# Performance work log

Measured on AMD Instinct MI355X. Metric: run time of the kernel, lower is better.

Reference implementation:

```python
import jax, jax.numpy as jnp
import numpy as np

C = 512          # pc_feat_dim == model_channels
NPTS = 5000      # points per sample (hard-coded in source reshape)
BO = 32          # number of samples
P = 20           # parts per sample (all valid)
S = BO * P       # total valid parts / segments = 640
PPP = (BO * NPTS) // S   # points per part = 250
T = BO * NPTS    # total points = 160000
NUM_FREQS = 10


def setup_inputs() -> dict:
    key = jax.random.key(0)
    ks = jax.random.split(key, 16)
    w = lambda k, shp: (jax.random.normal(k, shp, jnp.float32) * 0.02)
    return {
        "noise_param": jax.random.normal(ks[0], (S, 7), jnp.float32),
        "timesteps": jax.random.randint(ks[1], (BO,), 0, 1000, dtype=jnp.int32),
        "part_pcs": jax.random.normal(ks[2], (T, 3), jnp.float32),
        "segment_ids": (jnp.arange(T, dtype=jnp.int32) // PPP),
        "batch_length": jnp.full((S,), PPP, dtype=jnp.int32),
        "pe_w": w(ks[3], (3, C)), "pe_b": jnp.zeros((C,), jnp.float32),
        "t_w1": w(ks[4], (C, C)), "t_b1": jnp.zeros((C,), jnp.float32),
        "t_w2": w(ks[5], (C, C)), "t_b2": jnp.zeros((C,), jnp.float32),
        "pfc_w": w(ks[6], (147, C)), "pfc_b": jnp.zeros((C,), jnp.float32),
        "o_w1": w(ks[7], (C, 256)), "o_b1": jnp.zeros((256,), jnp.float32),
        "bn1_g": jnp.ones((256,), jnp.float32), "bn1_b": jnp.zeros((256,), jnp.float32),
        "o_w2": w(ks[8], (256, 128)), "o_b2": jnp.zeros((128,), jnp.float32),
        "bn2_g": jnp.ones((128,), jnp.float32), "bn2_b": jnp.zeros((128,), jnp.float32),
        "o_w3": w(ks[9], (128, 7)), "o_b3": jnp.zeros((7,), jnp.float32),
    }


def quat_apply(q, p):
    # pytorch3d convention: quaternion real-part-first (w, x, y, z)
    w, v = q[..., :1], q[..., 1:]
    t = 2.0 * jnp.cross(v, p)
    return p + w * t + jnp.cross(v, t)


def timestep_embedding(t, dim):
    half = dim // 2
    freqs = jnp.exp(-jnp.log(10000.0) * jnp.arange(half, dtype=jnp.float32) / half)
    args = t.astype(jnp.float32)[:, None] * freqs[None, :]
    return jnp.concatenate([jnp.cos(args), jnp.sin(args)], axis=-1)


def nerf_embed(x):
    # include_input, log-sampled freqs 2^0..2^9, fns (sin, cos) -> 7*(1+20)=147
    bands = 2.0 ** jnp.arange(NUM_FREQS, dtype=jnp.float32)
    xb = x[:, None, :] * bands[None, :, None]              # [S, F, 7]
    sc = jnp.concatenate([jnp.sin(xb), jnp.cos(xb)], -1)   # [S, F, 14]
    return jnp.concatenate([x, sc.reshape(x.shape[0], -1)], axis=-1)  # [S, 147]


def batchnorm(x, g, b):
    # training-mode BatchNorm1d over batch dim, eps 1e-5 (biased variance)
    m = x.mean(axis=0)
    v = x.var(axis=0)
    return (x - m) * jax.lax.rsqrt(v + 1e-5) * g + b


def reference(noise_param, timesteps, part_pcs, segment_ids, batch_length,
              pe_w, pe_b, t_w1, t_b1, t_w2, t_b2, pfc_w, pfc_b,
              o_w1, o_b1, bn1_g, bn1_b, o_w2, o_b2, bn2_g, bn2_b, o_w3, o_b3):
    # per-part quaternion + translation, applied per-point via gather
    quat = noise_param[:, 3:]
    quat = quat / jnp.linalg.norm(quat, axis=-1, keepdims=True)
    trans = noise_param[:, :3]
    pts = quat_apply(quat[segment_ids], part_pcs) + trans[segment_ids]  # [T, 3]

    # time embedding MLP (Linear -> SiLU -> Linear), per sample
    temb = timestep_embedding(timesteps, C)
    temb = jax.nn.silu(temb @ t_w1 + t_b1) @ t_w2 + t_b2                # [BO, C]

    feats = pts @ pe_w + pe_b                                           # [T, C]
    point_batch = jnp.arange(T, dtype=jnp.int32) // NPTS
    feats = feats + temb[point_batch]

    # per-part param embedding broadcast-added to that part's points
    pemb = nerf_embed(noise_param) @ pfc_w + pfc_b                      # [S, C]
    feats = feats + pemb[segment_ids]

    # (PointTransformer self/cross layers treated as identity)

    # ragged segment mean pooling
    pooled = jax.ops.segment_sum(feats, segment_ids, num_segments=S)
    pooled = pooled / batch_length[:, None].astype(pooled.dtype)        # [S, C]

    # out head (dropout off)
    h = jax.nn.relu(batchnorm(pooled @ o_w1 + o_b1, bn1_g, bn1_b))
    h = jax.nn.relu(batchnorm(h @ o_w2 + o_b2, bn2_g, bn2_b))
    return h @ o_w3 + o_b3                                              # [S, 7]
```

## Files before the change

kernel.cpp:

```cpp
#include <hip/hip_runtime.h>
#include <math.h>

#define NF 147
#define NBP 152

__global__ __launch_bounds__(256) void k1(
    const float* __restrict__ noise, const int* __restrict__ tsteps,
    const float* __restrict__ pcs, const int* __restrict__ bl,
    const float* __restrict__ t_w1, const float* __restrict__ t_b1,
    const float* __restrict__ t_w2, const float* __restrict__ t_b2,
    const float* __restrict__ pe_w, const float* __restrict__ pe_b,
    const float* __restrict__ pfc_w, const float* __restrict__ pfc_b,
    const float* __restrict__ o_w1,
    float* __restrict__ h1, float* __restrict__ WM, float* __restrict__ nb,
    int* __restrict__ statsz)
{
    __shared__ float shm[6144];
    __shared__ float np7s[4][8];
    __shared__ float wsum[4][3];
    __shared__ float rms[4][3];
    int blk = blockIdx.x, tid = threadIdx.x;

    if (blk < 128) {
        int b = blk >> 2, jq = blk & 3;
        float tf = (float)tsteps[b];
        float f = expf(-9.210340371976184f * (float)tid * (1.f / 256.f));
        float sn, cs;
        sincosf(tf * f, &sn, &cs);
        shm[tid] = cs; shm[256 + tid] = sn;
        __syncthreads();
        int jj = tid & 127, j = jq * 128 + jj;
        int ks = tid >> 7, k0 = ks << 8;
        float acc = 0.f;
        #pragma unroll 8
        for (int k = k0; k < k0 + 256; k++) acc += shm[k] * t_w1[k * 512 + j];
        shm[512 + ks * 128 + jj] = acc;
        __syncthreads();
        if (tid < 128) {
            float v = shm[512 + tid] + shm[640 + tid] + t_b1[jq * 128 + tid];
            h1[b * 512 + jq * 128 + tid] = v / (1.f + expf(-v));
        }
    } else if (blk < 294) {
        int m = blk - 128, r4 = m * 4;
        float* srcs = shm;
        float* red  = shm + 2048;
        #pragma unroll
        for (int q = 0; q < 2; q++) {
            int idx = tid + q * 256;
            int row = idx >> 7;
            int off4 = (idx & 127) << 2;
            int kr = r4 + row;
            float4 v;
            if (kr < 512)      v = *(const float4*)&t_w2[(size_t)kr * 512 + off4];
            else if (kr < 659) v = *(const float4*)&pfc_w[(size_t)(kr - 512) * 512 + off4];
            else if (kr < 662) v = *(const float4*)&pe_w[(size_t)(kr - 659) * 512 + off4];
            else if (kr == 662) {
                float4 a = *(const float4*)&pe_b[off4];
                float4 bq = *(const float4*)&pfc_b[off4];
                v.x = a.x + bq.x; v.y = a.y + bq.y; v.z = a.z + bq.z; v.w = a.w + bq.w;
            } else v = *(const float4*)&t_b2[off4];
            *(float4*)&srcs[row * 512 + off4] = v;
        }
        __syncthreads();
        int ks = tid >> 6, c4 = (tid & 63) << 2;
        float4 acc[4];
        #pragma unroll
        for (int i = 0; i < 4; i++) acc[i] = make_float4(0.f, 0.f, 0.f, 0.f);
        int j0 = ks * 128;
        #pragma unroll 4
        for (int jj = 0; jj < 128; jj++) {
            int j = j0 + jj;
            float4 w = *(const float4*)&o_w1[j * 256 + c4];
            #pragma unroll
            for (int i = 0; i < 4; i++) {
                float s = srcs[i * 512 + j];
                acc[i].x += s * w.x; acc[i].y += s * w.y;
                acc[i].z += s * w.z; acc[i].w += s * w.w;
            }
        }
        #pragma unroll
        for (int i = 0; i < 4; i++) *(float4*)&red[(ks * 4 + i) * 256 + c4] = acc[i];
        __syncthreads();
        #pragma unroll
        for (int t = 0; t < 4; t++) {
            int o = tid + t * 256;
            int i = o >> 8, c = o & 255;
            WM[(size_t)(r4 + i) * 256 + c] = red[i * 256 + c] + red[(4 + i) * 256 + c]
                                           + red[(8 + i) * 256 + c] + red[(12 + i) * 256 + c];
        }
    } else if (blk < 454) {
        int blkg = blk - 294;
        int s0 = blkg * 4;
        {
            const float4* p4 = (const float4*)(pcs + (size_t)blkg * 3000);
            #pragma unroll
            for (int i = 0; i < 3; i++) {
                int idx = tid + i * 256;
                if (idx < 750) *(float4*)&shm[idx * 4] = p4[idx];
            }
        }
        if (tid < 28) np7s[tid / 7][tid % 7] = noise[s0 * 7 + tid];
        __syncthreads();
        int w = tid >> 6, lane = tid & 63;
        {
            float sx = 0.f, sy = 0.f, sz = 0.f;
            const float* base = shm + w * 750;
            #pragma unroll
            for (int it = 0; it < 4; it++) {
                int q = lane + it * 64;
                if (q < 250) {
                    sx += base[q * 3 + 0];
                    sy += base[q * 3 + 1];
                    sz += base[q * 3 + 2];
                }
            }
            for (int off = 32; off >= 1; off >>= 1) {
                sx += __shfl_down(sx, off, 64);
                sy += __shfl_down(sy, off, 64);
                sz += __shfl_down(sz, off, 64);
            }
            if (lane == 0) { wsum[w][0] = sx; wsum[w][1] = sy; wsum[w][2] = sz; }
        }
        __syncthreads();
        if (tid < 4) {
            float inv = 1.f / (float)bl[s0 + tid];
            float mx = wsum[tid][0] * inv, my = wsum[tid][1] * inv, mz = wsum[tid][2] * inv;
            float qw = np7s[tid][3], qx = np7s[tid][4], qy = np7s[tid][5], qz = np7s[tid][6];
            float qn = rsqrtf(qw * qw + qx * qx + qy * qy + qz * qz);
            qw *= qn; qx *= qn; qy *= qn; qz *= qn;
            float tx = 2.f * (qy * mz - qz * my);
            float ty = 2.f * (qz * mx - qx * mz);
            float tz = 2.f * (qx * my - qy * mx);
            float r0 = mx + qw * tx + (qy * tz - qz * ty) + np7s[tid][0];
            float r1 = my + qw * ty + (qz * tx - qx * tz) + np7s[tid][1];
            float r2 = mz + qw * tz + (qx * ty - qy * tx) + np7s[tid][2];
            nb[(size_t)(s0 + tid) * NBP + 148] = r0;
            nb[(size_t)(s0 + tid) * NBP + 149] = r1;
            nb[(size_t)(s0 + tid) * NBP + 150] = r2;
        }
        for (int u = tid; u < 4 * NF; u += 256) {
            int r = u / NF, f = u % NF;
            float v;
            if (f < 7) v = np7s[r][f];
            else {
                int j = f - 7;
                int fi = j / 14, x = j % 14;
                float band = (float)(1 << fi);
                v = (x < 7) ? sinf(np7s[r][x] * band) : cosf(np7s[r][x - 7] * band);
            }
            nb[(size_t)(s0 + r) * NBP + f] = v;
        }
    } else {
        for (int z = tid; z < 772; z += 256) statsz[z] = 0;
    }
}

__global__ __launch_bounds__(256) void k2(
    const float* __restrict__ o_b1,
    const float* __restrict__ h1, const float* __restrict__ WM,
    const float* __restrict__ nb,
    float* __restrict__ g1, float* __restrict__ tg)
{
    __shared__ float shm[1024];
    int blk = blockIdx.x, tid = threadIdx.x;

    if (blk < 160) {
        int s0 = blk * 4;
        if (tid < 152) {
            ((float4*)shm)[tid] = ((const float4*)(nb + (size_t)s0 * NBP))[tid];
        }
        __syncthreads();
        int c = tid;
        float b0 = WM[662 * 256 + c];
        float a0 = b0, a1 = b0, a2 = b0, a3 = b0;
        #pragma unroll 7
        for (int f = 0; f < NF; f++) {
            float wv = WM[(512 + f) * 256 + c];
            a0 += shm[f] * wv;
            a1 += shm[NBP + f] * wv;
            a2 += shm[2 * NBP + f] * wv;
            a3 += shm[3 * NBP + f] * wv;
        }
        #pragma unroll
        for (int d = 0; d < 3; d++) {
            float wv = WM[(659 + d) * 256 + c];
            a0 += shm[148 + d] * wv;
            a1 += shm[NBP + 148 + d] * wv;
            a2 += shm[2 * NBP + 148 + d] * wv;
            a3 += shm[3 * NBP + 148 + d] * wv;
        }
        g1[(s0 + 0) * 256 + c] = a0;
        g1[(s0 + 1) * 256 + c] = a1;
        g1[(s0 + 2) * 256 + c] = a2;
        g1[(s0 + 3) * 256 + c] = a3;
    } else {
        int q = blk - 160;
        int b = q >> 2, cq = q & 3;
        shm[tid] = h1[b * 512 + tid];
        shm[256 + tid] = h1[b * 512 + 256 + tid];
        __syncthreads();
        int ks = tid >> 6, cc = tid & 63;
        int c = cq * 64 + cc;
        int k0 = ks * 128;
        float acc = 0.f;
        #pragma unroll 8
        for (int k = k0; k < k0 + 128; k++) acc += shm[k] * WM[k * 256 + c];
        shm[512 + ks * 64 + cc] = acc;
        __syncthreads();
        if (tid < 64) {
            int c2 = cq * 64 + tid;
            tg[b * 256 + c2] = shm[512 + tid] + shm[576 + tid] + shm[640 + tid]
                             + shm[704 + tid] + WM[663 * 256 + c2] + o_b1[c2];
        }
    }
}

__global__ __launch_bounds__(128) void kCD(
    const float* __restrict__ g1, const float* __restrict__ tg,
    float* __restrict__ stats1,
    const float* __restrict__ bn1_g, const float* __restrict__ bn1_b,
    const float* __restrict__ o_w2, const float* __restrict__ o_b2,
    const float* __restrict__ bn2_g, const float* __restrict__ bn2_b,
    const float* __restrict__ o_w3, const float* __restrict__ o_b3,
    float* __restrict__ stats2, int* __restrict__ cntA, int* __restrict__ cntB,
    float* __restrict__ out)
{
    int blk = blockIdx.x, tid = threadIdx.x;
    int r0 = blk * 8;
    __shared__ float rows[8][256];
    __shared__ float scale[256], shift[256];
    __shared__ float rowsB[8][128];
    __shared__ float w3[128 * 7];

    #pragma unroll
    for (int w = 0; w < 4; w++) {
        int idx4 = (tid + w * 128) << 2;
        int r = idx4 >> 8, c = idx4 & 255;
        int s = r0 + r;
        float4 gv = *(const float4*)&g1[s * 256 + c];
        float4 tv = *(const float4*)&tg[(s / 20) * 256 + c];
        gv.x += tv.x; gv.y += tv.y; gv.z += tv.z; gv.w += tv.w;
        *(float4*)&rows[r][c] = gv;
    }
    for (int i = tid; i < 128 * 7; i += 128) w3[i] = o_w3[i];
    __syncthreads();
    for (int c = tid; c < 256; c += 128) {
        float sm = 0.f, ss = 0.f;
        #pragma unroll
        for (int r = 0; r < 8; r++) { float x = rows[r][c]; sm += x; ss += x * x; }
        atomicAdd(&stats1[c], sm);
        atomicAdd(&stats1[256 + c], ss);
    }

    __syncthreads();
    if (tid == 0) {
        __threadfence();
        atomicAdd(cntA, 1);
        while (atomicAdd(cntA, 0) < 80) { }
        __threadfence();
    }
    __syncthreads();

    for (int c = tid; c < 256; c += 128) {
        float m = stats1[c] * (1.f / 640.f);
        float v = stats1[256 + c] * (1.f / 640.f) - m * m;
        float sc = rsqrtf(v + 1e-5f) * bn1_g[c];
        scale[c] = sc;
        shift[c] = bn1_b[c] - m * sc;
    }
    __syncthreads();
    for (int i = tid; i < 2048; i += 128) {
        int r = i >> 8, c = i & 255;
        float x = rows[r][c] * scale[c] + shift[c];
        rows[r][c] = x > 0.f ? x : 0.f;
    }
    __syncthreads();

    float acc[8];
    float bb = o_b2[tid];
    #pragma unroll
    for (int r = 0; r < 8; r++) acc[r] = bb;
    #pragma unroll 8
    for (int k = 0; k < 256; k++) {
        float w = o_w2[k * 128 + tid];
        #pragma unroll
        for (int r = 0; r < 8; r++) acc[r] += rows[r][k] * w;
    }
    float sm = 0.f, ss = 0.f;
    #pragma unroll
    for (int r = 0; r < 8; r++) { sm += acc[r]; ss += acc[r] * acc[r]; }
    atomicAdd(&stats2[tid], sm);
    atomicAdd(&stats2[128 + tid], ss);

    __syncthreads();
    if (tid == 0) {
        __threadfence();
        atomicAdd(cntB, 1);
        while (atomicAdd(cntB, 0) < 80) { }
        __threadfence();
    }
    __syncthreads();

    {
        float m = stats2[tid] * (1.f / 640.f);
        float v = stats2[128 + tid] * (1.f / 640.f) - m * m;
        float sc = rsqrtf(v + 1e-5f) * bn2_g[tid];
        float sh2 = bn2_b[tid] - m * sc;
        #pragma unroll
        for (int r = 0; r < 8; r++) {
            float x = acc[r] * sc + sh2;
            rowsB[r][tid] = x > 0.f ? x : 0.f;
        }
    }
    __syncthreads();
    if (tid < 56) {
        int r = tid / 7, j = tid % 7;
        float a3 = o_b3[j];
        #pragma unroll 8
        for (int k = 0; k < 128; k++) a3 += rowsB[r][k] * w3[k * 7 + j];
        out[(r0 + r) * 7 + j] = a3;
    }
}

extern "C" void kernel_launch(void* const* d_in, const int* in_sizes, int n_in,
                              void* d_out, int out_size, void* d_ws, size_t ws_size,
                              hipStream_t stream) {
    const float* noise = (const float*)d_in[0];
    const int* tsteps = (const int*)d_in[1];
    const float* pcs = (const float*)d_in[2];
    const int* bl = (const int*)d_in[4];
    const float* pe_w = (const float*)d_in[5];
    const float* pe_b = (const float*)d_in[6];
    const float* t_w1 = (const float*)d_in[7];
    const float* t_b1 = (const float*)d_in[8];
    const float* t_w2 = (const float*)d_in[9];
    const float* t_b2 = (const float*)d_in[10];
    const float* pfc_w = (const float*)d_in[11];
    const float* pfc_b = (const float*)d_in[12];
    const float* o_w1 = (const float*)d_in[13];
    const float* o_b1 = (const float*)d_in[14];
    const float* bn1_g = (const float*)d_in[15];
    const float* bn1_b = (const float*)d_in[16];
    const float* o_w2 = (const float*)d_in[17];
    const float* o_b2 = (const float*)d_in[18];
    const float* bn2_g = (const float*)d_in[19];
    const float* bn2_b = (const float*)d_in[20];
    const float* o_w3 = (const float*)d_in[21];
    const float* o_b3 = (const float*)d_in[22];

    float* ws = (float*)d_ws;
    float* h1    = ws + 0;
    float* WM    = ws + 16384;
    float* nb    = ws + 186368;
    float* g1    = ws + 283648;
    float* tg    = ws + 447488;
    float* stats = ws + 455680;
    int*   cnt   = (int*)(ws + 456448);

    k1<<<455, 256, 0, stream>>>(noise, tsteps, pcs, bl, t_w1, t_b1, t_w2, t_b2,
                                pe_w, pe_b, pfc_w, pfc_b, o_w1,
                                h1, WM, nb, (int*)stats);
    k2<<<288, 256, 0, stream>>>(o_b1, h1, WM, nb, g1, tg);
    kCD<<<80, 128, 0, stream>>>(g1, tg, stats, bn1_g, bn1_b, o_w2, o_b2,
                                bn2_g, bn2_b, o_w3, o_b3,
                                stats + 512, cnt, cnt + 1, (float*)d_out);
}
```

Baseline: 146.9 us.

## Fuse k2 projection into kCD and widen kCD to 256 threads

Removes the separate k2 launch by computing the per-batch time projection and the per-part feature projection inside kCD, so the g1/tg intermediates are never written to global memory. kCD now runs 256 threads and splits the o_w2 matmul K dimension over two halves, with a shared-memory reduction. This saves a kernel launch and a global round trip. In exchange, each of the 80 blocks recomputes a 512x256 time projection for up to two batches (redundant work), and the pre-barrier phase is longer on only 80 blocks, which reduces parallelism compared with the 288-block k2.

```diff
diff --git a/kernel.cpp b/kernel.cpp
--- a/kernel.cpp
+++ b/kernel.cpp
@@ -18,7 +18,6 @@
     __shared__ float shm[6144];
     __shared__ float np7s[4][8];
     __shared__ float wsum[4][3];
-    __shared__ float rms[4][3];
     int blk = blockIdx.x, tid = threadIdx.x;
 
     if (blk < 128) {
@@ -131,12 +130,9 @@
             float tx = 2.f * (qy * mz - qz * my);
             float ty = 2.f * (qz * mx - qx * mz);
             float tz = 2.f * (qx * my - qy * mx);
-            float r0 = mx + qw * tx + (qy * tz - qz * ty) + np7s[tid][0];
-            float r1 = my + qw * ty + (qz * tx - qx * tz) + np7s[tid][1];
-            float r2 = mz + qw * tz + (qx * ty - qy * tx) + np7s[tid][2];
-            nb[(size_t)(s0 + tid) * NBP + 148] = r0;
-            nb[(size_t)(s0 + tid) * NBP + 149] = r1;
-            nb[(size_t)(s0 + tid) * NBP + 150] = r2;
+            nb[(size_t)(s0 + tid) * NBP + 148] = mx + qw * tx + (qy * tz - qz * ty) + np7s[tid][0];
+            nb[(size_t)(s0 + tid) * NBP + 149] = my + qw * ty + (qz * tx - qx * tz) + np7s[tid][1];
+            nb[(size_t)(s0 + tid) * NBP + 150] = mz + qw * tz + (qx * ty - qy * tx) + np7s[tid][2];
         }
         for (int u = tid; u < 4 * NF; u += 256) {
             int r = u / NF, f = u % NF;
@@ -155,68 +151,9 @@
     }
 }
 
-__global__ __launch_bounds__(256) void k2(
-    const float* __restrict__ o_b1,
+__global__ __launch_bounds__(256) void kCD(
     const float* __restrict__ h1, const float* __restrict__ WM,
-    const float* __restrict__ nb,
-    float* __restrict__ g1, float* __restrict__ tg)
-{
-    __shared__ float shm[1024];
-    int blk = blockIdx.x, tid = threadIdx.x;
-
-    if (blk < 160) {
-        int s0 = blk * 4;
-        if (tid < 152) {
-            ((float4*)shm)[tid] = ((const float4*)(nb + (size_t)s0 * NBP))[tid];
-        }
-        __syncthreads();
-        int c = tid;
-        float b0 = WM[662 * 256 + c];
-        float a0 = b0, a1 = b0, a2 = b0, a3 = b0;
-        #pragma unroll 7
-        for (int f = 0; f < NF; f++) {
-            float wv = WM[(512 + f) * 256 + c];
-            a0 += shm[f] * wv;
-            a1 += shm[NBP + f] * wv;
-            a2 += shm[2 * NBP + f] * wv;
-            a3 += shm[3 * NBP + f] * wv;
-        }
-        #pragma unroll
-        for (int d = 0; d < 3; d++) {
-            float wv = WM[(659 + d) * 256 + c];
-            a0 += shm[148 + d] * wv;
-            a1 += shm[NBP + 148 + d] * wv;
-            a2 += shm[2 * NBP + 148 + d] * wv;
-            a3 += shm[3 * NBP + 148 + d] * wv;
-        }
-        g1[(s0 + 0) * 256 + c] = a0;
-        g1[(s0 + 1) * 256 + c] = a1;
-        g1[(s0 + 2) * 256 + c] = a2;
-        g1[(s0 + 3) * 256 + c] = a3;
-    } else {
-        int q = blk - 160;
-        int b = q >> 2, cq = q & 3;
-        shm[tid] = h1[b * 512 + tid];
-        shm[256 + tid] = h1[b * 512 + 256 + tid];
-        __syncthreads();
-        int ks = tid >> 6, cc = tid & 63;
-        int c = cq * 64 + cc;
-        int k0 = ks * 128;
-        float acc = 0.f;
-        #pragma unroll 8
-        for (int k = k0; k < k0 + 128; k++) acc += shm[k] * WM[k * 256 + c];
-        shm[512 + ks * 64 + cc] = acc;
-        __syncthreads();
-        if (tid < 64) {
-            int c2 = cq * 64 + tid;
-            tg[b * 256 + c2] = shm[512 + tid] + shm[576 + tid] + shm[640 + tid]
-                             + shm[704 + tid] + WM[663 * 256 + c2] + o_b1[c2];
-        }
-    }
-}
-
-__global__ __launch_bounds__(128) void kCD(
-    const float* __restrict__ g1, const float* __restrict__ tg,
+    const float* __restrict__ nb, const float* __restrict__ o_b1,
     float* __restrict__ stats1,
     const float* __restrict__ bn1_g, const float* __restrict__ bn1_b,
     const float* __restrict__ o_w2, const float* __restrict__ o_b2,
@@ -225,29 +162,72 @@
     float* __restrict__ stats2, int* __restrict__ cntA, int* __restrict__ cntB,
     float* __restrict__ out)
 {
+    __shared__ float nbs[1216];
+    __shared__ float hr[1024];
+    __shared__ float tgl[512];
+    __shared__ float rows[2048];
+    __shared__ float scale[256], shift[256];
+    __shared__ float rowsB[1024];
+    __shared__ float w3s[896];
+    __shared__ float red2[2048];
+
     int blk = blockIdx.x, tid = threadIdx.x;
     int r0 = blk * 8;
-    __shared__ float rows[8][256];
-    __shared__ float scale[256], shift[256];
-    __shared__ float rowsB[8][128];
-    __shared__ float w3[128 * 7];
-
-    #pragma unroll
-    for (int w = 0; w < 4; w++) {
-        int idx4 = (tid + w * 128) << 2;
-        int r = idx4 >> 8, c = idx4 & 255;
-        int s = r0 + r;
-        float4 gv = *(const float4*)&g1[s * 256 + c];
-        float4 tv = *(const float4*)&tg[(s / 20) * 256 + c];
-        gv.x += tv.x; gv.y += tv.y; gv.z += tv.z; gv.w += tv.w;
-        *(float4*)&rows[r][c] = gv;
-    }
-    for (int i = tid; i < 128 * 7; i += 128) w3[i] = o_w3[i];
-    __syncthreads();
-    for (int c = tid; c < 256; c += 128) {
+    int b0 = r0 / 20;
+    int b1 = (r0 + 7) / 20;
+
+    for (int i = tid; i < 304; i += 256)
+        ((float4*)nbs)[i] = ((const float4*)(nb + (size_t)r0 * NBP))[i];
+    {
+        int i = tid;
+        hr[i] = h1[b0 * 512 + i];
+        hr[256 + i] = h1[b0 * 512 + 256 + i];
+        hr[512 + i] = h1[b1 * 512 + i];
+        hr[768 + i] = h1[b1 * 512 + 256 + i];
+    }
+    for (int i = tid; i < 896; i += 256) w3s[i] = o_w3[i];
+    __syncthreads();
+
+    {
+        int c = tid;
+        float a0 = 0.f, a1 = 0.f;
+        #pragma unroll 8
+        for (int k = 0; k < 512; k++) {
+            float wv = WM[k * 256 + c];
+            a0 += hr[k] * wv;
+            a1 += hr[512 + k] * wv;
+        }
+        float base = WM[663 * 256 + c] + o_b1[c];
+        tgl[c] = a0 + base;
+        tgl[256 + c] = a1 + base;
+    }
+    __syncthreads();
+
+    {
+        int c = tid;
+        float a[8];
+        float bcst = WM[662 * 256 + c];
+        #pragma unroll
+        for (int r = 0; r < 8; r++) a[r] = bcst;
+        #pragma unroll 7
+        for (int f = 0; f < NF; f++) {
+            float wv = WM[(512 + f) * 256 + c];
+            #pragma unroll
+            for (int r = 0; r < 8; r++) a[r] += nbs[r * NBP + f] * wv;
+        }
+        #pragma unroll
+        for (int d = 0; d < 3; d++) {
+            float wv = WM[(659 + d) * 256 + c];
+            #pragma unroll
+            for (int r = 0; r < 8; r++) a[r] += nbs[r * NBP + 148 + d] * wv;
+        }
         float sm = 0.f, ss = 0.f;
         #pragma unroll
-        for (int r = 0; r < 8; r++) { float x = rows[r][c]; sm += x; ss += x * x; }
+        for (int r = 0; r < 8; r++) {
+            float x = a[r] + tgl[((r0 + r) / 20 - b0) * 256 + c];
+            rows[r * 256 + c] = x;
+            sm += x; ss += x * x;
+        }
         atomicAdd(&stats1[c], sm);
         atomicAdd(&stats1[256 + c], ss);
     }
@@ -261,36 +241,50 @@
     }
     __syncthreads();
 
-    for (int c = tid; c < 256; c += 128) {
-        float m = stats1[c] * (1.f / 640.f);
-        float v = stats1[256 + c] * (1.f / 640.f) - m * m;
-        float sc = rsqrtf(v + 1e-5f) * bn1_g[c];
-        scale[c] = sc;
-        shift[c] = bn1_b[c] - m * sc;
-    }
-    __syncthreads();
-    for (int i = tid; i < 2048; i += 128) {
+    {
+        float m = stats1[tid] * (1.f / 640.f);
+        float v = stats1[256 + tid] * (1.f / 640.f) - m * m;
+        float sc = rsqrtf(v + 1e-5f) * bn1_g[tid];
+        scale[tid] = sc;
+        shift[tid] = bn1_b[tid] - m * sc;
+    }
+    __syncthreads();
+    for (int i = tid; i < 2048; i += 256) {
         int r = i >> 8, c = i & 255;
-        float x = rows[r][c] * scale[c] + shift[c];
-        rows[r][c] = x > 0.f ? x : 0.f;
-    }
-    __syncthreads();
-
-    float acc[8];
-    float bb = o_b2[tid];
-    #pragma unroll
-    for (int r = 0; r < 8; r++) acc[r] = bb;
-    #pragma unroll 8
-    for (int k = 0; k < 256; k++) {
-        float w = o_w2[k * 128 + tid];
-        #pragma unroll
-        for (int r = 0; r < 8; r++) acc[r] += rows[r][k] * w;
-    }
-    float sm = 0.f, ss = 0.f;
-    #pragma unroll
-    for (int r = 0; r < 8; r++) { sm += acc[r]; ss += acc[r] * acc[r]; }
-    atomicAdd(&stats2[tid], sm);
-    atomicAdd(&stats2[128 + tid], ss);
+        float x = rows[r * 256 + c] * scale[c] + shift[c];
+        rows[r * 256 + c] = x > 0.f ? x : 0.f;
+    }
+    __syncthreads();
+
+    {
+        int ks = tid >> 7, c2 = tid & 127;
+        float acc[8];
+        #pragma unroll
+        for (int r = 0; r < 8; r++) acc[r] = 0.f;
+        int kb = ks * 128;
+        #pragma unroll 8
+        for (int kk = 0; kk < 128; kk++) {
+            int k = kb + kk;
+            float w = o_w2[k * 128 + c2];
+            #pragma unroll
+            for (int r = 0; r < 8; r++) acc[r] += rows[r * 256 + k] * w;
+        }
+        #pragma unroll
+        for (int r = 0; r < 8; r++) red2[(ks * 8 + r) * 128 + c2] = acc[r];
+    }
+    __syncthreads();
+    if (tid < 128) {
+        float bb = o_b2[tid];
+        float sm = 0.f, ss = 0.f;
+        #pragma unroll
+        for (int r = 0; r < 8; r++) {
+            float h = red2[r * 128 + tid] + red2[(8 + r) * 128 + tid] + bb;
+            rowsB[r * 128 + tid] = h;
+            sm += h; ss += h * h;
+        }
+        atomicAdd(&stats2[tid], sm);
+        atomicAdd(&stats2[128 + tid], ss);
+    }
 
     __syncthreads();
     if (tid == 0) {
@@ -301,24 +295,24 @@
     }
     __syncthreads();
 
-    {
+    if (tid < 128) {
         float m = stats2[tid] * (1.f / 640.f);
         float v = stats2[128 + tid] * (1.f / 640.f) - m * m;
         float sc = rsqrtf(v + 1e-5f) * bn2_g[tid];
-        float sh2 = bn2_b[tid] - m * sc;
+        float sh = bn2_b[tid] - m * sc;
         #pragma unroll
         for (int r = 0; r < 8; r++) {
-            float x = acc[r] * sc + sh2;
-            rowsB[r][tid] = x > 0.f ? x : 0.f;
+            float x = rowsB[r * 128 + tid] * sc + sh;
+            rowsB[r * 128 + tid] = x > 0.f ? x : 0.f;
         }
     }
     __syncthreads();
     if (tid < 56) {
-        int r = tid / 7, j = tid % 7;
-        float a3 = o_b3[j];
+        int r = tid / 7, jo = tid % 7;
+        float a3 = o_b3[jo];
         #pragma unroll 8
-        for (int k = 0; k < 128; k++) a3 += rowsB[r][k] * w3[k * 7 + j];
-        out[(r0 + r) * 7 + j] = a3;
+        for (int k = 0; k < 128; k++) a3 += rowsB[r * 128 + k] * w3s[k * 7 + jo];
+        out[(r0 + r) * 7 + jo] = a3;
     }
 }
 
@@ -352,16 +346,13 @@
     float* h1    = ws + 0;
     float* WM    = ws + 16384;
     float* nb    = ws + 186368;
-    float* g1    = ws + 283648;
-    float* tg    = ws + 447488;
-    float* stats = ws + 455680;
-    int*   cnt   = (int*)(ws + 456448);
+    float* stats = ws + 283648;
+    int*   cnt   = (int*)(ws + 284416);
 
     k1<<<455, 256, 0, stream>>>(noise, tsteps, pcs, bl, t_w1, t_b1, t_w2, t_b2,
                                 pe_w, pe_b, pfc_w, pfc_b, o_w1,
                                 h1, WM, nb, (int*)stats);
-    k2<<<288, 256, 0, stream>>>(o_b1, h1, WM, nb, g1, tg);
-    kCD<<<80, 128, 0, stream>>>(g1, tg, stats, bn1_g, bn1_b, o_w2, o_b2,
-                                bn2_g, bn2_b, o_w3, o_b3,
+    kCD<<<80, 256, 0, stream>>>(h1, WM, nb, o_b1, stats, bn1_g, bn1_b,
+                                o_w2, o_b2, bn2_g, bn2_b, o_w3, o_b3,
                                 stats + 512, cnt, cnt + 1, (float*)d_out);
 }
```

After: 184.7 us. 25.8% more time.

## Retile weight-folding GEMM blocks to 8 rows by half the output columns

Applied to the files above, without the earlier changes.

Each block in the fused weight-premultiply section (t_w2/pfc_w/pe_w rows times o_w1) now handles 8 source rows and one 128-column half of the output, instead of 4 rows across all 256 columns. The block count stays the same, but each o_w1 element read from global memory is reused across 8 rows instead of 4, and each thread accumulates 8 float2 values. Shared memory grows to hold the larger source tile and the reduction buffer, which may lower occupancy, and the o_w1 loads become float2 instead of float4. A small unused shared array is removed and some temporaries are inlined.

```diff
diff --git a/kernel.cpp b/kernel.cpp
--- a/kernel.cpp
+++ b/kernel.cpp
@@ -15,10 +15,9 @@
     float* __restrict__ h1, float* __restrict__ WM, float* __restrict__ nb,
     int* __restrict__ statsz)
 {
-    __shared__ float shm[6144];
+    __shared__ float shm[8192];
     __shared__ float np7s[4][8];
     __shared__ float wsum[4][3];
-    __shared__ float rms[4][3];
     int blk = blockIdx.x, tid = threadIdx.x;
 
     if (blk < 128) {
@@ -41,15 +40,17 @@
             h1[b * 512 + jq * 128 + tid] = v / (1.f + expf(-v));
         }
     } else if (blk < 294) {
-        int m = blk - 128, r4 = m * 4;
+        int m = blk - 128;
+        int rg = m >> 1, ch = m & 1;
+        int r8 = rg * 8;
         float* srcs = shm;
-        float* red  = shm + 2048;
-        #pragma unroll
-        for (int q = 0; q < 2; q++) {
+        float* red  = shm + 4096;
+        #pragma unroll
+        for (int q = 0; q < 4; q++) {
             int idx = tid + q * 256;
             int row = idx >> 7;
             int off4 = (idx & 127) << 2;
-            int kr = r4 + row;
+            int kr = r8 + row;
             float4 v;
             if (kr < 512)      v = *(const float4*)&t_w2[(size_t)kr * 512 + off4];
             else if (kr < 659) v = *(const float4*)&pfc_w[(size_t)(kr - 512) * 512 + off4];
@@ -62,31 +63,33 @@
             *(float4*)&srcs[row * 512 + off4] = v;
         }
         __syncthreads();
-        int ks = tid >> 6, c4 = (tid & 63) << 2;
-        float4 acc[4];
-        #pragma unroll
-        for (int i = 0; i < 4; i++) acc[i] = make_float4(0.f, 0.f, 0.f, 0.f);
+        int ks = tid >> 6, lane = tid & 63;
+        int cbase = ch * 128 + lane * 2;
+        float2 acc[8];
+        #pragma unroll
+        for (int i = 0; i < 8; i++) { acc[i].x = 0.f; acc[i].y = 0.f; }
         int j0 = ks * 128;
         #pragma unroll 4
         for (int jj = 0; jj < 128; jj++) {
             int j = j0 + jj;
-            float4 w = *(const float4*)&o_w1[j * 256 + c4];
+            float2 w = *(const float2*)&o_w1[j * 256 + cbase];
             #pragma unroll
-            for (int i = 0; i < 4; i++) {
+            for (int i = 0; i < 8; i++) {
                 float s = srcs[i * 512 + j];
                 acc[i].x += s * w.x; acc[i].y += s * w.y;
-                acc[i].z += s * w.z; acc[i].w += s * w.w;
-            }
-        }
-        #pragma unroll
-        for (int i = 0; i < 4; i++) *(float4*)&red[(ks * 4 + i) * 256 + c4] = acc[i];
+            }
+        }
+        #pragma unroll
+        for (int i = 0; i < 8; i++)
+            *(float2*)&red[(ks * 8 + i) * 128 + lane * 2] = acc[i];
         __syncthreads();
         #pragma unroll
         for (int t = 0; t < 4; t++) {
             int o = tid + t * 256;
-            int i = o >> 8, c = o & 255;
-            WM[(size_t)(r4 + i) * 256 + c] = red[i * 256 + c] + red[(4 + i) * 256 + c]
-                                           + red[(8 + i) * 256 + c] + red[(12 + i) * 256 + c];
+            int i = o >> 7, c = o & 127;
+            WM[(size_t)(r8 + i) * 256 + ch * 128 + c] =
+                red[i * 128 + c] + red[(8 + i) * 128 + c]
+              + red[(16 + i) * 128 + c] + red[(24 + i) * 128 + c];
         }
     } else if (blk < 454) {
         int blkg = blk - 294;
@@ -131,12 +134,9 @@
             float tx = 2.f * (qy * mz - qz * my);
             float ty = 2.f * (qz * mx - qx * mz);
             float tz = 2.f * (qx * my - qy * mx);
-            float r0 = mx + qw * tx + (qy * tz - qz * ty) + np7s[tid][0];
-            float r1 = my + qw * ty + (qz * tx - qx * tz) + np7s[tid][1];
-            float r2 = mz + qw * tz + (qx * ty - qy * tx) + np7s[tid][2];
-            nb[(size_t)(s0 + tid) * NBP + 148] = r0;
-            nb[(size_t)(s0 + tid) * NBP + 149] = r1;
-            nb[(size_t)(s0 + tid) * NBP + 150] = r2;
+            nb[(size_t)(s0 + tid) * NBP + 148] = mx + qw * tx + (qy * tz - qz * ty) + np7s[tid][0];
+            nb[(size_t)(s0 + tid) * NBP + 149] = my + qw * ty + (qz * tx - qx * tz) + np7s[tid][1];
+            nb[(size_t)(s0 + tid) * NBP + 150] = mz + qw * tz + (qx * ty - qy * tx) + np7s[tid][2];
         }
         for (int u = tid; u < 4 * NF; u += 256) {
             int r = u / NF, f = u % NF;
```

Result: no change. 148.5 us (+1.1%).
